# Performance work log

Hardware: AMD Instinct MI355X
Metric: run time of the kernel (lower is better)

The kernel has to match this reference:

```python
import jax, jax.numpy as jnp
import numpy as np

N_NODES = 50000
N_EDGES = 200000
NODE_DIM = 160     # node feat dim (divisible by 5 per wrapper slicing)
EDGE_DIM = 64      # latent edge feat dim
RAW_EDGE_DIM = 8   # raw geometric edge attributes
HID = 256          # hidden dim of edge/node update MLPs
ENC_HID = 128      # hidden dim of EASP edge encoder
N_ITER = 3
ENC_IN = 2 * NODE_DIM + RAW_EDGE_DIM                 # 328
EDGE_IN = 2 * 2 * NODE_DIM + 2 * EDGE_DIM            # 768 (reattach -> factor 2)
MSG_IN = 2 * NODE_DIM + EDGE_DIM                     # 384 (reattach node + edge)


def _ln(x, g, b):
    mu = jnp.mean(x, axis=-1, keepdims=True)
    v = jnp.var(x, axis=-1, keepdims=True)
    return (x - mu) * jax.lax.rsqrt(v + 1e-5) * g + b


def setup_inputs() -> dict:
    key = jax.random.key(0)
    ks = jax.random.split(key, 24)

    def w(k, shape):
        return (jax.random.normal(k, shape, jnp.float32) / np.sqrt(shape[0])).astype(jnp.float32)

    return {
        'x': jax.random.normal(ks[0], (N_NODES, NODE_DIM), jnp.float32),
        'edge_attr': jax.random.normal(ks[1], (N_EDGES, RAW_EDGE_DIM), jnp.float32),
        # EASP edge encoder MLP
        'enc_W1': w(ks[2], (ENC_IN, ENC_HID)), 'enc_b1': jnp.zeros((ENC_HID,), jnp.float32),
        'enc_W2': w(ks[3], (ENC_HID, EDGE_DIM)), 'enc_b2': jnp.zeros((EDGE_DIM,), jnp.float32),
        # EdgeCNN edge update MLP
        'eW1': w(ks[4], (EDGE_IN, HID)), 'eb1': jnp.zeros((HID,), jnp.float32),
        'eW2': w(ks[5], (HID, EDGE_DIM)), 'eb2': jnp.zeros((EDGE_DIM,), jnp.float32),
        # AttentionNodeUpdateNet: per-edge message MLP + attention vector + node out
        'mW1': w(ks[6], (MSG_IN, HID)), 'mb1': jnp.zeros((HID,), jnp.float32),
        'att_v': w(ks[7], (HID,)),
        'nW1': w(ks[8], (HID, NODE_DIM)), 'nb1': jnp.zeros((NODE_DIM,), jnp.float32),
        # shared LayerNorms (ModuleList([layer]*n_iter) shares one layer)
        'ln_ng': jnp.ones((NODE_DIM,), jnp.float32), 'ln_nb': jnp.zeros((NODE_DIM,), jnp.float32),
        'ln_eg': jnp.ones((EDGE_DIM,), jnp.float32), 'ln_eb': jnp.zeros((EDGE_DIM,), jnp.float32),
        'edge_row': jax.random.randint(ks[9], (N_EDGES,), 0, N_NODES, jnp.int32),
        'edge_col': jax.random.randint(ks[10], (N_EDGES,), 0, N_NODES, jnp.int32),
    }


def reference(x, edge_attr, enc_W1, enc_b1, enc_W2, enc_b2, eW1, eb1, eW2, eb2,
              mW1, mb1, att_v, nW1, nb1, ln_ng, ln_nb, ln_eg, ln_eb,
              edge_row, edge_col):
    row, col = edge_row, edge_col
    # edge encoder: gather endpoints, encode raw edge attrs
    init_edge = jnp.concatenate([x[row], x[col], edge_attr], axis=1)  # [E, 328]
    init_edge = jnp.maximum(init_edge @ enc_W1 + enc_b1, 0.0) @ enc_W2 + enc_b2  # [E, 64]

    node_lat, edge_lat = x, init_edge
    for _ in range(N_ITER):
        nl = jnp.concatenate([x, node_lat], axis=1)            # reattach initial node feats [N, 320]
        el = jnp.concatenate([init_edge, edge_lat], axis=1)    # reattach initial edge feats [E, 128]
        # edge update: gather-concat-MLP
        e_in = jnp.concatenate([nl[row], nl[col], el], axis=1)  # [E, 768]
        new_edge = jnp.maximum(e_in @ eW1 + eb1, 0.0) @ eW2 + eb2  # [E, 64]
        # node update: per-edge message + segment-softmax attention + scatter agg
        msg = jnp.maximum(jnp.concatenate([nl[col], new_edge], axis=1) @ mW1 + mb1, 0.0)  # [E, 256]
        logit = jax.nn.leaky_relu(msg @ att_v, 0.2)             # [E]
        smax = jax.ops.segment_max(logit, row, num_segments=N_NODES)
        ex = jnp.exp(logit - smax[row])
        den = jax.ops.segment_sum(ex, row, num_segments=N_NODES)
        alpha = ex / (den[row] + 1e-16)
        agg = jax.ops.segment_sum(alpha[:, None] * msg, row, num_segments=N_NODES)  # [N, 256]
        new_node = agg @ nW1 + nb1                              # [N, 160]
        # residual skip + (shared) LayerNorm
        node_lat = _ln(x + new_node, ln_ng, ln_nb)
        edge_lat = _ln(init_edge + new_edge, ln_eg, ln_eb)
    return node_lat, edge_lat
```

## Files before the change

### kernel.cpp

```cpp
#include <hip/hip_runtime.h>
#include <stdint.h>

#define N_NODES 50000
#define N_EDGES 200000
#define SCAN_B 512

typedef __bf16 bf16_t;
typedef bf16_t bf16x8 __attribute__((ext_vector_type(8)));
typedef float f32x4 __attribute__((ext_vector_type(4)));

__device__ __forceinline__ float bf2f(ushort h) {
  union { unsigned int u; float f; } c; c.u = ((unsigned int)h) << 16; return c.f;
}
__device__ __forceinline__ ushort f2bf(float f) {
  union { float f; unsigned int u; } c; c.f = f;
  unsigned int r = (c.u >> 16) & 1u;
  c.u += 0x7fffu + r;
  return (ushort)(c.u >> 16);
}
__device__ __forceinline__ float wave_sum(float v) {
#pragma unroll
  for (int m = 32; m > 0; m >>= 1) v += __shfl_xor(v, m, 64);
  return v;
}

__global__ void detect_k(const ushort* x, unsigned int* flag) {
  int i = blockIdx.x * 256 + threadIdx.x;
  unsigned int cnt = 0;
  for (int j = i; j < 1000000; j += 64 * 256) {
    ushort v = x[j];
    if (((v & 0x7F80u) == 0x7F80u) && (v & 0x7Fu)) cnt++;
  }
  if (cnt) atomicAdd(flag, cnt);
}

__global__ void cvt_in_k(const void* src, ushort* dst, int n, const unsigned int* flag) {
  int i = blockIdx.x * 256 + threadIdx.x;
  if (i >= n) return;
  if (*flag >= 2) dst[i] = f2bf(((const float*)src)[i]);
  else            dst[i] = ((const ushort*)src)[i];
}

__global__ void cvt_eattr_k(const void* src, const int* perm, ushort* dst,
                            const unsigned int* flag) {
  int i = blockIdx.x * 256 + threadIdx.x;
  if (i >= N_EDGES * 8) return;
  int e = i >> 3, j = i & 7;
  size_t o = (size_t)perm[e] * 8 + j;
  if (*flag >= 2) dst[i] = f2bf(((const float*)src)[o]);
  else            dst[i] = ((const ushort*)src)[o];
}

__global__ void transpose2_k(const void* W, ushort* Bt, int k0, int Ksrc, int Kpad,
                             int Wstride, const unsigned int* flag) {
  int k = blockIdx.x * 256 + threadIdx.x;
  int n = blockIdx.y;
  if (k >= Kpad) return;
  ushort v = 0;
  if (k < Ksrc) {
    if (*flag >= 2) v = f2bf(((const float*)W)[(size_t)(k0 + k) * Wstride + n]);
    else            v = ((const ushort*)W)[(size_t)(k0 + k) * Wstride + n];
  }
  Bt[(size_t)n * Kpad + k] = v;
}

__global__ void hist_k(const int* row, int* deg) {
  int e = blockIdx.x * 256 + threadIdx.x;
  if (e < N_EDGES) atomicAdd(&deg[row[e]], 1);
}
__global__ void scan_blk_k(const int* deg, int* off, int* bsum, int n) {
  __shared__ int s[SCAN_B];
  int i = blockIdx.x * SCAN_B + threadIdx.x;
  int v = (i < n) ? deg[i] : 0;
  s[threadIdx.x] = v;
  __syncthreads();
  for (int o = 1; o < SCAN_B; o <<= 1) {
    int t = (threadIdx.x >= o) ? s[threadIdx.x - o] : 0;
    __syncthreads();
    s[threadIdx.x] += t;
    __syncthreads();
  }
  if (i < n) off[i] = s[threadIdx.x] - v;
  if (threadIdx.x == SCAN_B - 1) bsum[blockIdx.x] = s[SCAN_B - 1];
}
__global__ void scan_top_k(int* bsum, int nb) {
  __shared__ int s[128];
  int v = (threadIdx.x < nb) ? bsum[threadIdx.x] : 0;
  s[threadIdx.x] = v;
  __syncthreads();
  for (int o = 1; o < 128; o <<= 1) {
    int t = (threadIdx.x >= o) ? s[threadIdx.x - o] : 0;
    __syncthreads();
    s[threadIdx.x] += t;
    __syncthreads();
  }
  if (threadIdx.x < nb) bsum[threadIdx.x] = s[threadIdx.x] - v;
}
__global__ void scan_add_k(int* off, const int* bsum, int n) {
  int i = blockIdx.x * 256 + threadIdx.x;
  if (i < n) off[i] += bsum[i >> 9];
  if (i == 0) off[n] = N_EDGES;
}
__global__ void fill_k(const int* row, const int* off, int* cur, int* perm) {
  int e = blockIdx.x * 256 + threadIdx.x;
  if (e >= N_EDGES) return;
  int r = row[e];
  int p = off[r] + atomicAdd(&cur[r], 1);
  perm[p] = e;
}
__global__ void gather_rc_k(const int* row, const int* col, const int* perm,
                            int* rs, int* cs) {
  int e = blockIdx.x * 256 + threadIdx.x;
  if (e >= N_EDGES) return;
  int o = perm[e];
  rs[e] = row[o];
  cs[e] = col[o];
}

struct GemmP {
  const ushort* X;
  const ushort* L;
  const ushort* E2;
  const float*  Af;
  const int* row;
  const int* col;
  const ushort* Bt;
  const ushort* bias;
  const ushort* Cr;
  const ushort* Cc;
  long cst;
  ushort* outb;  long ob_stride;
  ushort* outb2; long ob2_stride;
  ushort* outS;  long oS_stride;
  int nsplit;
  float*  outf;  long of_stride;
  long e2s;
  int M, K, Nw;
  int swzn;
};

template <int MODE>
__device__ __forceinline__ uint4 load_a8(const GemmP& p, int e, int kg) {
  if (MODE == 0) {
    return *(const uint4*)(p.E2 + (size_t)e * p.e2s + kg);
  } else if (MODE == 5) {
    if (kg < 160) return *(const uint4*)(p.X + (size_t)e * 160 + kg);
    return *(const uint4*)(p.L + (size_t)e * 160 + (kg - 160));
  } else if (MODE == 7) {
    if (kg < 160) return *(const uint4*)(p.X + (size_t)e * 160 + kg);
    uint4 z; z.x = z.y = z.z = z.w = 0u; return z;
  } else if (MODE == 8) {
    if (kg < 8) return *(const uint4*)(p.E2 + (size_t)e * 8);
    uint4 z; z.x = z.y = z.z = z.w = 0u; return z;
  } else {
    const float* s = p.Af + (size_t)e * p.K + kg;
    f32x4 f0 = *(const f32x4*)s;
    f32x4 f1 = *(const f32x4*)(s + 4);
    union { ushort r[8]; uint4 u; } o;
    o.r[0] = f2bf(f0[0]); o.r[1] = f2bf(f0[1]); o.r[2] = f2bf(f0[2]); o.r[3] = f2bf(f0[3]);
    o.r[4] = f2bf(f1[0]); o.r[5] = f2bf(f1[1]); o.r[6] = f2bf(f1[2]); o.r[7] = f2bf(f1[3]);
    return o.u;
  }
}

template <int MODE, int CI, bool RELU, int NT, bool LNN>
__global__ __launch_bounds__(256) void gemm_k(GemmP p) {
  constexpr int BR = NT / 2;
  constexpr int NTC = NT * 16;
  constexpr int CIP = NTC + 8;
  __shared__ __align__(16) ushort smem[9216 + 1152 * NT];
  ushort* Asm = smem;
  ushort* Bsm = smem + 9216;
  const int t = threadIdx.x;
  const int w = t >> 6;
  const int l = t & 63;
  int m0, n0;
  if (p.swzn) {
    int b = blockIdx.x;
    int panel = (b & 7) + ((b >> 3) / p.swzn) * 8;
    int nb = (b >> 3) % p.swzn;
    if (panel * 128 >= p.M) return;
    m0 = panel * 128;
    n0 = nb * NTC;
  } else {
    m0 = blockIdx.y * 128;
    n0 = blockIdx.x * NTC;
  }

  const int srow = t >> 1;
  const int sph = (t & 1) << 5;
  int e = m0 + srow;
  if (e >= p.M) e = p.M - 1;

  int bn_[BR], bk_[BR];
#pragma unroll
  for (int j = 0; j < BR; j++) {
    int cid = j * 256 + t;
    bn_[j] = cid >> 3;
    bk_[j] = (cid & 7) << 3;
  }

  const int mq = l & 15;
  const int qd = l >> 4;

  uint4 ar[4];
  uint4 br[BR];
  auto load_tile = [&](int k0) {
#pragma unroll
    for (int j = 0; j < 4; j++)
      ar[j] = load_a8<MODE>(p, e, k0 + sph + j * 8);
#pragma unroll
    for (int j = 0; j < BR; j++)
      br[j] = *(const uint4*)(p.Bt + (size_t)(n0 + bn_[j]) * p.K + k0 + bk_[j]);
  };

  load_tile(0);

  f32x4 acc[2][NT] = {};
  if (CI) {
#pragma unroll
    for (int mt = 0; mt < 2; mt++) {
#pragma unroll
      for (int i = 0; i < 4; i++) {
        int r = m0 + w * 32 + mt * 16 + qd * 4 + i;
        if (r >= p.M) r = p.M - 1;
        const ushort* pc = p.Cc + (size_t)p.col[r] * p.cst + n0 + mq;
        const ushort* pr = nullptr;
        if (CI == 1) pr = p.Cr + (size_t)p.row[r] * p.cst + n0 + mq;
#pragma unroll
        for (int nt = 0; nt < NT; nt++) {
          float v = bf2f(pc[nt * 16]);
          if (CI == 1) v += bf2f(pr[nt * 16]);
          acc[mt][nt][i] = v;
        }
      }
    }
  }

  const int kiters = p.K >> 6;
  for (int kt = 0; kt < kiters; kt++) {
    __syncthreads();
#pragma unroll
    for (int j = 0; j < 4; j++)
      *(uint4*)&Asm[srow * 72 + sph + j * 8] = ar[j];
#pragma unroll
    for (int j = 0; j < BR; j++)
      *(uint4*)&Bsm[bn_[j] * 72 + bk_[j]] = br[j];
    if (kt + 1 < kiters) load_tile((kt + 1) << 6);
    __syncthreads();
#pragma unroll
    for (int ph = 0; ph < 2; ph++) {
      uint4 ra0 = *(const uint4*)&Asm[(w * 32 + mq) * 72 + ph * 32 + qd * 8];
      uint4 ra1 = *(const uint4*)&Asm[(w * 32 + 16 + mq) * 72 + ph * 32 + qd * 8];
      bf16x8 af0 = __builtin_bit_cast(bf16x8, ra0);
      bf16x8 af1 = __builtin_bit_cast(bf16x8, ra1);
#pragma unroll
      for (int nt = 0; nt < NT; nt++) {
        uint4 rb = *(const uint4*)&Bsm[(nt * 16 + mq) * 72 + ph * 32 + qd * 8];
        bf16x8 bfv = __builtin_bit_cast(bf16x8, rb);
        acc[0][nt] = __builtin_amdgcn_mfma_f32_16x16x32_bf16(af0, bfv, acc[0][nt], 0, 0, 0);
        acc[1][nt] = __builtin_amdgcn_mfma_f32_16x16x32_bf16(af1, bfv, acc[1][nt], 0, 0, 0);
      }
    }
  }

  if (MODE == 4) {
    if (LNN) {
#pragma unroll
      for (int mt = 0; mt < 2; mt++) {
#pragma unroll
        for (int i = 0; i < 4; i++) {
          int r = m0 + w * 32 + mt * 16 + qd * 4 + i;
          int rc = (r < p.M) ? r : p.M - 1;
          float vals[NT];
          float s = 0.0f;
#pragma unroll
          for (int nt = 0; nt < NT; nt++) {
            int c = n0 + nt * 16 + mq;
            float v = acc[mt][nt][i] + bf2f(p.bias[c]) +
                      bf2f(p.X[(size_t)rc * p.of_stride + c]);
            vals[nt] = v; s += v;
          }
#pragma unroll
          for (int m = 1; m <= 8; m <<= 1) s += __shfl_xor(s, m, 64);
          float mu = s * (1.0f / 160.0f);
          float ss = 0.0f;
#pragma unroll
          for (int nt = 0; nt < NT; nt++) { float d = vals[nt] - mu; ss += d * d; }
#pragma unroll
          for (int m = 1; m <= 8; m <<= 1) ss += __shfl_xor(ss, m, 64);
          float inv = rsqrtf(ss * (1.0f / 160.0f) + 1e-5f);
          if (r < p.M) {
#pragma unroll
            for (int nt = 0; nt < NT; nt++) {
              int c = n0 + nt * 16 + mq;
              float o = (vals[nt] - mu) * inv * bf2f(p.Cr[c]) + bf2f(p.Cc[c]);
              p.outb[(size_t)r * p.ob_stride + c] = f2bf(o);
            }
          }
        }
      }
    } else {
#pragma unroll
      for (int mt = 0; mt < 2; mt++) {
#pragma unroll
        for (int nt = 0; nt < NT; nt++) {
          int c = n0 + nt * 16 + mq;
          float bv = bf2f(p.bias[c]);
#pragma unroll
          for (int i = 0; i < 4; i++) {
            int r = m0 + w * 32 + mt * 16 + qd * 4 + i;
            if (r >= p.M) continue;
            float v = acc[mt][nt][i] + bv;
            if (RELU) v = fmaxf(v, 0.0f);
            p.outf[(size_t)r * p.of_stride + c] = v;
          }
        }
      }
    }
  } else {
    ushort* dst = p.outb;
    long dstr = p.ob_stride;
    int nb0 = n0;
    if (p.outS && n0 >= p.nsplit) { dst = p.outS; dstr = p.oS_stride; nb0 = n0 - p.nsplit; }
    __syncthreads();
    ushort* S = smem + w * (32 * CIP);
#pragma unroll
    for (int mt = 0; mt < 2; mt++) {
#pragma unroll
      for (int nt = 0; nt < NT; nt++) {
        float bv = bf2f(p.bias[n0 + nt * 16 + mq]);
#pragma unroll
        for (int i = 0; i < 4; i++) {
          float v = acc[mt][nt][i] + bv;
          if (RELU) v = fmaxf(v, 0.0f);
          S[(mt * 16 + qd * 4 + i) * CIP + nt * 16 + mq] = f2bf(v);
        }
      }
    }
    __syncthreads();
#pragma unroll
    for (int j = 0; j < NT; j++) {
      int flat = (j * 64 + l) * 8;
      int lr = flat / NTC, cc = flat % NTC;
      int r = m0 + w * 32 + lr;
      if (r < p.M) {
        uint4 v = *(const uint4*)&S[lr * CIP + cc];
        *(uint4*)(dst + (size_t)r * dstr + nb0 + cc) = v;
        if (p.outb2) *(uint4*)(p.outb2 + (size_t)r * p.ob2_stride + n0 + cc) = v;
      }
    }
  }
}

__global__ __launch_bounds__(512) void edge12_k(
    const ushort* el, const int* rs, const int* cs, const ushort* Prc,
    const ushort* BtWe, const ushort* eb1, const ushort* Bte2, const ushort* eb2,
    ushort* elw, int M) {
  __shared__ __align__(16) ushort smem[32768];
  ushort* Asm = smem;
  ushort* Bsm = smem + 9216;
  const int t = threadIdx.x;
  const int w = t >> 6;
  const int l = t & 63;
  const int m0 = blockIdx.x * 128;
  const int mq = l & 15;
  const int qd = l >> 4;

  const int arow = t >> 2;
  const int aph = (t & 3) << 4;
  int ea = m0 + arow;
  if (ea >= M) ea = M - 1;
  int bn_[4], bk_[4];
#pragma unroll
  for (int j = 0; j < 4; j++) {
    int cid = j * 512 + t;
    bn_[j] = cid >> 3;
    bk_[j] = (cid & 7) << 3;
  }

  uint4 ar[2], br[4];
  auto load_tile = [&](int k0) {
#pragma unroll
    for (int j = 0; j < 2; j++)
      ar[j] = *(const uint4*)(el + (size_t)ea * 128 + k0 + aph + j * 8);
#pragma unroll
    for (int j = 0; j < 4; j++)
      br[j] = *(const uint4*)(BtWe + (size_t)bn_[j] * 128 + k0 + bk_[j]);
  };
  load_tile(0);

  f32x4 acc[16] = {};
#pragma unroll
  for (int i = 0; i < 4; i++) {
    int r = m0 + w * 16 + qd * 4 + i;
    if (r >= M) r = M - 1;
    const ushort* pc = Prc + (size_t)cs[r] * 512 + 256 + mq;
    const ushort* pr = Prc + (size_t)rs[r] * 512 + mq;
#pragma unroll
    for (int nt = 0; nt < 16; nt++)
      acc[nt][i] = bf2f(pc[nt * 16]) + bf2f(pr[nt * 16]);
  }

#pragma unroll
  for (int kt = 0; kt < 2; kt++) {
    __syncthreads();
#pragma unroll
    for (int j = 0; j < 2; j++)
      *(uint4*)&Asm[arow * 72 + aph + j * 8] = ar[j];
#pragma unroll
    for (int j = 0; j < 4; j++)
      *(uint4*)&Bsm[bn_[j] * 72 + bk_[j]] = br[j];
    if (kt == 0) load_tile(64);
    __syncthreads();
#pragma unroll
    for (int ph = 0; ph < 2; ph++) {
      uint4 ra = *(const uint4*)&Asm[(w * 16 + mq) * 72 + ph * 32 + qd * 8];
      bf16x8 af = __builtin_bit_cast(bf16x8, ra);
#pragma unroll
      for (int nt = 0; nt < 16; nt++) {
        uint4 rb = *(const uint4*)&Bsm[(nt * 16 + mq) * 72 + ph * 32 + qd * 8];
        bf16x8 bfv = __builtin_bit_cast(bf16x8, rb);
        acc[nt] = __builtin_amdgcn_mfma_f32_16x16x32_bf16(af, bfv, acc[nt], 0, 0, 0);
      }
    }
  }

  __syncthreads();
  ushort* S = smem + w * 4096;
#pragma unroll
  for (int nt = 0; nt < 16; nt++) {
    float bv = bf2f(eb1[nt * 16 + mq]);
#pragma unroll
    for (int i = 0; i < 4; i++) {
      int row = qd * 4 + i;
      float v = fmaxf(acc[nt][i] + bv, 0.0f);
      int bcol = ((nt * 16 + mq) * 2) ^ ((row & 7) << 4);
      S[row * 256 + (bcol >> 1)] = f2bf(v);
    }
  }
  __syncthreads();

  f32x4 acc2[4] = {};
#pragma unroll
  for (int ks = 0; ks < 8; ks++) {
    int bco = ((ks * 32 + qd * 8) * 2) ^ ((mq & 7) << 4);
    uint4 ra2 = *(const uint4*)&S[mq * 256 + (bco >> 1)];
    bf16x8 af2 = __builtin_bit_cast(bf16x8, ra2);
#pragma unroll
    for (int nt2 = 0; nt2 < 4; nt2++) {
      uint4 rb2 = *(const uint4*)(Bte2 + (size_t)(nt2 * 16 + mq) * 256 + ks * 32 + qd * 8);
      bf16x8 bf2v = __builtin_bit_cast(bf16x8, rb2);
      acc2[nt2] = __builtin_amdgcn_mfma_f32_16x16x32_bf16(af2, bf2v, acc2[nt2], 0, 0, 0);
    }
  }
  __syncthreads();

  ushort* S2 = smem + w * 1152;
#pragma unroll
  for (int nt2 = 0; nt2 < 4; nt2++) {
    float bv2 = bf2f(eb2[nt2 * 16 + mq]);
#pragma unroll
    for (int i = 0; i < 4; i++)
      S2[(qd * 4 + i) * 72 + nt2 * 16 + mq] = f2bf(acc2[nt2][i] + bv2);
  }
  __syncthreads();
#pragma unroll
  for (int j = 0; j < 2; j++) {
    int flat = (j * 64 + l) * 8;
    int lr = flat >> 6, cc = flat & 63;
    int r = m0 + w * 16 + lr;
    if (r < M)
      *(uint4*)(elw + (size_t)r * 128 + 64 + cc) = *(const uint4*)&S2[lr * 72 + cc];
  }
}

__global__ void copy_u4_k(const uint4* s, uint4* d, int n) {
  int i = blockIdx.x * 256 + threadIdx.x;
  if (i < n) d[i] = s[i];
}

__global__ void agg_csr_k(const ushort* msg, const ushort* att, const int* off,
                          float* agg) {
  int n = blockIdx.x * 4 + (threadIdx.x >> 6);
  int l = threadIdx.x & 63;
  if (n >= N_NODES) return;
  const int s0 = off[n], s1 = off[n + 1];
  ushort4 av = *(const ushort4*)(att + l * 4);
  const float a0 = bf2f(av.x), a1 = bf2f(av.y), a2 = bf2f(av.z), a3 = bf2f(av.w);
  float maxl = -1e30f;
  for (int j = s0; j < s1; j++) {
    ushort4 m = *(const ushort4*)(msg + (size_t)j * 256 + l * 4);
    float d = bf2f(m.x) * a0 + bf2f(m.y) * a1 + bf2f(m.z) * a2 + bf2f(m.w) * a3;
    d = wave_sum(d);
    float lg = (d > 0.0f) ? d : 0.2f * d;
    maxl = fmaxf(maxl, lg);
  }
  float den = 0.0f;
  f32x4 acc = {0.0f, 0.0f, 0.0f, 0.0f};
  for (int j = s0; j < s1; j++) {
    ushort4 m = *(const ushort4*)(msg + (size_t)j * 256 + l * 4);
    float m0 = bf2f(m.x), m1 = bf2f(m.y), m2 = bf2f(m.z), m3 = bf2f(m.w);
    float d = m0 * a0 + m1 * a1 + m2 * a2 + m3 * a3;
    d = wave_sum(d);
    float lg = (d > 0.0f) ? d : 0.2f * d;
    float ex = __expf(lg - maxl);
    den += ex;
    acc[0] += ex * m0; acc[1] += ex * m1; acc[2] += ex * m2; acc[3] += ex * m3;
  }
  float inv = 1.0f / (den + 1e-16f);
  f32x4 o = {acc[0] * inv, acc[1] * inv, acc[2] * inv, acc[3] * inv};
  *(f32x4*)(agg + (size_t)n * 256 + l * 4) = o;
}

__global__ void ln_edge_k(const ushort* g, const ushort* b, ushort* el) {
  int e = blockIdx.x * 4 + (threadIdx.x >> 6);
  int l = threadIdx.x & 63;
  if (e >= N_EDGES) return;
  float v = bf2f(el[(size_t)e * 128 + l]) + bf2f(el[(size_t)e * 128 + 64 + l]);
  float mu = wave_sum(v) * (1.0f / 64.0f);
  float d = v - mu;
  float var = wave_sum(d * d) * (1.0f / 64.0f);
  float inv = rsqrtf(var + 1e-5f);
  el[(size_t)e * 128 + 64 + l] = f2bf(d * inv * bf2f(g[l]) + bf2f(b[l]));
}

__global__ void out_node_k(const ushort* nlat, void* out, const unsigned int* flag) {
  int i = blockIdx.x * 256 + threadIdx.x;
  if (i >= N_NODES * 160) return;
  if (*flag >= 2) ((float*)out)[i] = bf2f(nlat[i]);
  else            ((ushort*)out)[i] = nlat[i];
}
__global__ void out_edge_k(const ushort* el, const int* perm, void* out,
                           const unsigned int* flag) {
  int i = blockIdx.x * 256 + threadIdx.x;
  if (i >= N_EDGES * 64) return;
  int e = i >> 6, c = i & 63;
  ushort v = el[(size_t)e * 128 + 64 + c];
  size_t o = (size_t)N_NODES * 160 + (size_t)perm[e] * 64 + c;
  if (*flag >= 2) ((float*)out)[o] = bf2f(v);
  else            ((ushort*)out)[o] = v;
}

extern "C" void kernel_launch(void* const* d_in, const int* in_sizes, int n_in,
                              void* d_out, int out_size, void* d_ws, size_t ws_size,
                              hipStream_t stream) {
  const void* x_r     = d_in[0];
  const void* eattr_r = d_in[1];
  const void* encW1   = d_in[2];
  const void* encb1_r = d_in[3];
  const void* encW2   = d_in[4];
  const void* encb2_r = d_in[5];
  const void* eW1     = d_in[6];
  const void* eb1_r   = d_in[7];
  const void* eW2     = d_in[8];
  const void* eb2_r   = d_in[9];
  const void* mW1     = d_in[10];
  const void* mb1_r   = d_in[11];
  const void* attv_r  = d_in[12];
  const void* nW1     = d_in[13];
  const void* nb1_r   = d_in[14];
  const void* lnng_r  = d_in[15];
  const void* lnnb_r  = d_in[16];
  const void* lneg_r  = d_in[17];
  const void* lneb_r  = d_in[18];
  const int* erow = (const int*)d_in[19];
  const int* ecol = (const int*)d_in[20];
  (void)in_sizes; (void)n_in;

  char* ws = (char*)d_ws;
  size_t off = 0;
  auto alloc = [&](size_t bytes) -> void* {
    void* p = ws + off;
    off = (off + bytes + 511) & ~(size_t)511;
    return p;
  };
  ushort* hm   = (ushort*)alloc((size_t)N_EDGES * 256 * 2);
  ushort* el   = (ushort*)alloc((size_t)N_EDGES * 128 * 2);
  float*  agg  = (float*)alloc((size_t)N_NODES * 256 * 4);
  ushort* xc   = (ushort*)alloc((size_t)N_NODES * 160 * 2);
  ushort* nlat = (ushort*)alloc((size_t)N_NODES * 160 * 2);
  ushort* Qc   = (ushort*)alloc((size_t)N_NODES * 256 * 2);
  int* degcur  = (int*)alloc((size_t)2 * N_NODES * 4);
  int* offcsr  = (int*)alloc((size_t)(N_NODES + 1) * 4);
  int* perm    = (int*)alloc((size_t)N_EDGES * 4);
  int* rs      = (int*)alloc((size_t)N_EDGES * 4);
  int* cs      = (int*)alloc((size_t)N_EDGES * 4);
  int* bsum    = (int*)alloc((size_t)128 * 4);
  ushort* BtPe = (ushort*)alloc((size_t)256 * 192 * 2);
  ushort* BtWenc = (ushort*)alloc((size_t)128 * 64 * 2);
  ushort* BtE2 = (ushort*)alloc((size_t)64 * 128 * 2);
  ushort* BtPQ = (ushort*)alloc((size_t)768 * 320 * 2);
  ushort* BtWe = (ushort*)alloc((size_t)256 * 128 * 2);
  ushort* Bte2 = (ushort*)alloc((size_t)64 * 256 * 2);
  ushort* BtWm = (ushort*)alloc((size_t)256 * 64 * 2);
  ushort* Btn1 = (ushort*)alloc((size_t)160 * 256 * 2);
  ushort* pool = (ushort*)alloc((size_t)4096 * 2);
  unsigned int* flag = (unsigned int*)alloc(64);
  ushort* msg = hm;
  ushort* eac  = (ushort*)agg;
  ushort* Penc = (ushort*)((char*)agg + (size_t)N_EDGES * 8 * 2);
  ushort* Prc  = (ushort*)agg;
  ushort* zb   = pool + 2048;

  ushort* encb1c = pool;        ushort* encb2c = pool + 128;
  ushort* eb1c   = pool + 192;  ushort* eb2c   = pool + 448;
  ushort* mb1c   = pool + 512;  ushort* attvc  = pool + 768;
  ushort* nb1c   = pool + 1024; ushort* lnngc  = pool + 1184;
  ushort* lnnbc  = pool + 1344; ushort* lnegc  = pool + 1504;
  ushort* lnebc  = pool + 1568;

  if (off > ws_size) {
    hipMemsetAsync(d_out, 0, (size_t)out_size * 2, stream);
    return;
  }

  hipMemsetAsync(flag, 0, 64, stream);
  hipMemsetAsync(pool, 0, 4096 * 2, stream);
  hipMemsetAsync(degcur, 0, (size_t)2 * N_NODES * 4, stream);

  detect_k<<<64, 256, 0, stream>>>((const ushort*)x_r, flag);

  {
    int* deg = degcur;
    int* cur = degcur + N_NODES;
    const int nb = (N_NODES + SCAN_B - 1) / SCAN_B;
    hist_k<<<(N_EDGES + 255) / 256, 256, 0, stream>>>(erow, deg);
    scan_blk_k<<<nb, SCAN_B, 0, stream>>>(deg, offcsr, bsum, N_NODES);
    scan_top_k<<<1, 128, 0, stream>>>(bsum, nb);
    scan_add_k<<<(N_NODES + 255) / 256, 256, 0, stream>>>(offcsr, bsum, N_NODES);
    fill_k<<<(N_EDGES + 255) / 256, 256, 0, stream>>>(erow, offcsr, cur, perm);
    gather_rc_k<<<(N_EDGES + 255) / 256, 256, 0, stream>>>(erow, ecol, perm, rs, cs);
  }

  cvt_in_k<<<(N_NODES * 160 + 255) / 256, 256, 0, stream>>>(x_r, xc, N_NODES * 160, flag);
  cvt_eattr_k<<<(N_EDGES * 8 + 255) / 256, 256, 0, stream>>>(eattr_r, perm, eac, flag);
  cvt_in_k<<<1, 256, 0, stream>>>(encb1_r, encb1c, 128, flag);
  cvt_in_k<<<1, 256, 0, stream>>>(encb2_r, encb2c, 64, flag);
  cvt_in_k<<<1, 256, 0, stream>>>(eb1_r, eb1c, 256, flag);
  cvt_in_k<<<1, 256, 0, stream>>>(eb2_r, eb2c, 64, flag);
  cvt_in_k<<<1, 256, 0, stream>>>(mb1_r, mb1c, 256, flag);
  cvt_in_k<<<1, 256, 0, stream>>>(attv_r, attvc, 256, flag);
  cvt_in_k<<<1, 256, 0, stream>>>(nb1_r, nb1c, 160, flag);
  cvt_in_k<<<1, 256, 0, stream>>>(lnng_r, lnngc, 160, flag);
  cvt_in_k<<<1, 256, 0, stream>>>(lnnb_r, lnnbc, 160, flag);
  cvt_in_k<<<1, 256, 0, stream>>>(lneg_r, lnegc, 64, flag);
  cvt_in_k<<<1, 256, 0, stream>>>(lneb_r, lnebc, 64, flag);

  transpose2_k<<<dim3(1, 128), 256, 0, stream>>>(encW1, BtPe,             0, 160, 192, 128, flag);
  transpose2_k<<<dim3(1, 128), 256, 0, stream>>>(encW1, BtPe + 128 * 192, 160, 160, 192, 128, flag);
  transpose2_k<<<dim3(1, 128), 256, 0, stream>>>(encW1, BtWenc,           320, 8, 64, 128, flag);
  transpose2_k<<<dim3(1, 64), 256, 0, stream>>>(encW2, BtE2, 0, 128, 128, 64, flag);
  transpose2_k<<<dim3(2, 256), 256, 0, stream>>>(eW1, BtPQ,             0, 320, 320, 256, flag);
  transpose2_k<<<dim3(2, 256), 256, 0, stream>>>(eW1, BtPQ + 256 * 320, 320, 320, 320, 256, flag);
  transpose2_k<<<dim3(2, 256), 256, 0, stream>>>(mW1, BtPQ + 512 * 320, 0, 320, 320, 256, flag);
  transpose2_k<<<dim3(1, 256), 256, 0, stream>>>(eW1, BtWe, 640, 128, 128, 256, flag);
  transpose2_k<<<dim3(1, 64), 256, 0, stream>>>(eW2, Bte2, 0, 256, 256, 64, flag);
  transpose2_k<<<dim3(1, 256), 256, 0, stream>>>(mW1, BtWm, 320, 64, 64, 256, flag);
  transpose2_k<<<dim3(1, 160), 256, 0, stream>>>(nW1, Btn1, 0, 256, 256, 160, flag);

  copy_u4_k<<<(N_NODES * 160 / 8 + 255) / 256, 256, 0, stream>>>(
      (const uint4*)xc, (uint4*)nlat, N_NODES * 160 / 8);

  const int gE = (N_EDGES + 127) / 128;
  const int gN = (N_NODES + 127) / 128;
  const int gN8 = 8 * ((gN + 7) / 8);
  const int gE8 = 8 * ((gE + 7) / 8);

  {
    GemmP p{};
    p.X = xc; p.Bt = BtPe; p.bias = zb;
    p.outb = Penc; p.ob_stride = 256;
    p.M = N_NODES; p.K = 192; p.Nw = 256; p.swzn = 2;
    gemm_k<7, 0, false, 8, false><<<gN8 * 2, 256, 0, stream>>>(p);
  }
  {
    GemmP p{};
    p.E2 = eac; p.row = rs; p.col = cs;
    p.Cr = Penc; p.Cc = Penc + 128; p.cst = 256;
    p.Bt = BtWenc; p.bias = encb1c;
    p.outb = hm; p.ob_stride = 128;
    p.M = N_EDGES; p.K = 64; p.Nw = 128;
    gemm_k<8, 1, true, 8, false><<<dim3(1, gE), 256, 0, stream>>>(p);
  }
  {
    GemmP p{};
    p.E2 = hm; p.e2s = 128; p.Bt = BtE2; p.bias = encb2c;
    p.outb = el; p.ob_stride = 128;
    p.outb2 = el + 64; p.ob2_stride = 128;
    p.M = N_EDGES; p.K = 128; p.Nw = 64;
    gemm_k<0, 0, false, 4, false><<<dim3(1, gE), 256, 0, stream>>>(p);
  }

  for (int it = 0; it < 3; it++) {
    {
      GemmP p{};
      p.X = xc; p.L = nlat; p.Bt = BtPQ; p.bias = zb;
      p.outb = Prc; p.ob_stride = 512;
      p.outS = Qc; p.oS_stride = 256; p.nsplit = 512;
      p.M = N_NODES; p.K = 320; p.Nw = 768; p.swzn = 6;
      gemm_k<5, 0, false, 8, false><<<gN8 * 6, 256, 0, stream>>>(p);
    }
    edge12_k<<<gE, 512, 0, stream>>>(el, rs, cs, Prc, BtWe, eb1c, Bte2, eb2c,
                                     el, N_EDGES);
    {
      GemmP p{};
      p.E2 = el + 64; p.e2s = 128; p.row = rs; p.col = cs;
      p.Cc = Qc; p.cst = 256;
      p.Bt = BtWm; p.bias = mb1c;
      p.outb = msg; p.ob_stride = 256;
      p.M = N_EDGES; p.K = 64; p.Nw = 256; p.swzn = 2;
      gemm_k<0, 2, true, 8, false><<<gE8 * 2, 256, 0, stream>>>(p);
    }
    ln_edge_k<<<N_EDGES / 4, 256, 0, stream>>>(lnegc, lnebc, el);
    agg_csr_k<<<(N_NODES + 3) / 4, 256, 0, stream>>>(msg, attvc, offcsr, agg);
    {
      GemmP p{};
      p.Af = agg; p.Bt = Btn1; p.bias = nb1c;
      p.X = xc; p.of_stride = 160;
      p.Cr = lnngc; p.Cc = lnnbc;
      p.outb = nlat; p.ob_stride = 160;
      p.M = N_NODES; p.K = 256; p.Nw = 160;
      gemm_k<4, 0, false, 10, true><<<dim3(1, gN), 256, 0, stream>>>(p);
    }
  }

  out_node_k<<<(N_NODES * 160 + 255) / 256, 256, 0, stream>>>(nlat, d_out, flag);
  out_edge_k<<<(N_EDGES * 64 + 255) / 256, 256, 0, stream>>>(el, perm, d_out, flag);
  (void)out_size;
}
```

Measured before the change: 1.979 ms.

## Fuse message GEMM into edge MLP kernel and drop block swizzle

Merges the per-edge message GEMM (new_edge @ mW1 plus the gathered Q[col] term, bias and ReLU) into the edge-update kernel. The freshly computed new_edge tile is reused from shared memory instead of being written out and re-read by a separate GEMM launch. The XOR swizzle patterns are adjusted and the Q[col] gathers are issued early to overlap with the second GEMM. It also removes the panel block-swizzle in the generic GEMM and goes back to a plain 2D grid, which may hurt L2 reuse. The fused kernel needs more accumulator registers (16 extra f32x4), which may lower occupancy.

Measured after the change: 1.894 ms. -4.3%, faster.

```diff
diff --git a/kernel.cpp b/kernel.cpp
--- a/kernel.cpp
+++ b/kernel.cpp
@@ -136,7 +136,6 @@
   float*  outf;  long of_stride;
   long e2s;
   int M, K, Nw;
-  int swzn;
 };
 
 template <int MODE>
@@ -174,18 +173,8 @@
   const int t = threadIdx.x;
   const int w = t >> 6;
   const int l = t & 63;
-  int m0, n0;
-  if (p.swzn) {
-    int b = blockIdx.x;
-    int panel = (b & 7) + ((b >> 3) / p.swzn) * 8;
-    int nb = (b >> 3) % p.swzn;
-    if (panel * 128 >= p.M) return;
-    m0 = panel * 128;
-    n0 = nb * NTC;
-  } else {
-    m0 = blockIdx.y * 128;
-    n0 = blockIdx.x * NTC;
-  }
+  const int m0 = blockIdx.y * 128;
+  const int n0 = blockIdx.x * NTC;
 
   const int srow = t >> 1;
   const int sph = (t & 1) << 5;
@@ -353,10 +342,11 @@
   }
 }
 
-__global__ __launch_bounds__(512) void edge12_k(
+__global__ __launch_bounds__(512) void edge123_k(
     const ushort* el, const int* rs, const int* cs, const ushort* Prc,
-    const ushort* BtWe, const ushort* eb1, const ushort* Bte2, const ushort* eb2,
-    ushort* elw, int M) {
+    const ushort* Qc, const ushort* BtWe, const ushort* eb1,
+    const ushort* Bte2, const ushort* eb2, const ushort* BtWm,
+    const ushort* mb1, ushort* elw, ushort* msg, int M) {
   __shared__ __align__(16) ushort smem[32768];
   ushort* Asm = smem;
   ushort* Bsm = smem + 9216;
@@ -435,17 +425,26 @@
     for (int i = 0; i < 4; i++) {
       int row = qd * 4 + i;
       float v = fmaxf(acc[nt][i] + bv, 0.0f);
-      int bcol = ((nt * 16 + mq) * 2) ^ ((row & 7) << 4);
-      S[row * 256 + (bcol >> 1)] = f2bf(v);
-    }
+      S[row * 256 + ((nt * 16 + mq) ^ ((row & 15) << 3))] = f2bf(v);
+    }
+  }
+
+  f32x4 acc3[16];
+#pragma unroll
+  for (int i = 0; i < 4; i++) {
+    int r = m0 + w * 16 + qd * 4 + i;
+    if (r >= M) r = M - 1;
+    const ushort* pq = Qc + (size_t)cs[r] * 256 + mq;
+#pragma unroll
+    for (int nt = 0; nt < 16; nt++)
+      acc3[nt][i] = bf2f(pq[nt * 16]);
   }
   __syncthreads();
 
   f32x4 acc2[4] = {};
 #pragma unroll
   for (int ks = 0; ks < 8; ks++) {
-    int bco = ((ks * 32 + qd * 8) * 2) ^ ((mq & 7) << 4);
-    uint4 ra2 = *(const uint4*)&S[mq * 256 + (bco >> 1)];
+    uint4 ra2 = *(const uint4*)&S[mq * 256 + ((ks * 32 + qd * 8) ^ ((mq & 15) << 3))];
     bf16x8 af2 = __builtin_bit_cast(bf16x8, ra2);
 #pragma unroll
     for (int nt2 = 0; nt2 < 4; nt2++) {
@@ -456,22 +455,63 @@
   }
   __syncthreads();
 
-  ushort* S2 = smem + w * 1152;
+  ushort* Sne = smem + w * 1024;
 #pragma unroll
   for (int nt2 = 0; nt2 < 4; nt2++) {
     float bv2 = bf2f(eb2[nt2 * 16 + mq]);
 #pragma unroll
-    for (int i = 0; i < 4; i++)
-      S2[(qd * 4 + i) * 72 + nt2 * 16 + mq] = f2bf(acc2[nt2][i] + bv2);
+    for (int i = 0; i < 4; i++) {
+      int row = qd * 4 + i;
+      Sne[row * 64 + ((nt2 * 16 + mq) ^ ((row & 7) << 3))] = f2bf(acc2[nt2][i] + bv2);
+    }
   }
   __syncthreads();
-#pragma unroll
-  for (int j = 0; j < 2; j++) {
+
+  {
+    int row = l >> 2;
+    int r = m0 + w * 16 + row;
+#pragma unroll
+    for (int h = 0; h < 2; h++) {
+      int cbase = (l & 3) * 16 + h * 8;
+      if (r < M)
+        *(uint4*)(elw + (size_t)r * 128 + 64 + cbase) =
+            *(const uint4*)&Sne[row * 64 + (cbase ^ ((row & 7) << 3))];
+    }
+  }
+
+#pragma unroll
+  for (int ph = 0; ph < 2; ph++) {
+    uint4 ra3 = *(const uint4*)&Sne[mq * 64 + ((ph * 32 + qd * 8) ^ ((mq & 7) << 3))];
+    bf16x8 af3 = __builtin_bit_cast(bf16x8, ra3);
+#pragma unroll
+    for (int nt = 0; nt < 16; nt++) {
+      uint4 rb3 = *(const uint4*)(BtWm + (size_t)(nt * 16 + mq) * 64 + ph * 32 + qd * 8);
+      bf16x8 bf3v = __builtin_bit_cast(bf16x8, rb3);
+      acc3[nt] = __builtin_amdgcn_mfma_f32_16x16x32_bf16(af3, bf3v, acc3[nt], 0, 0, 0);
+    }
+  }
+  __syncthreads();
+
+#pragma unroll
+  for (int nt = 0; nt < 16; nt++) {
+    float bv3 = bf2f(mb1[nt * 16 + mq]);
+#pragma unroll
+    for (int i = 0; i < 4; i++) {
+      int row = qd * 4 + i;
+      float v = fmaxf(acc3[nt][i] + bv3, 0.0f);
+      S[row * 256 + ((nt * 16 + mq) ^ ((row & 15) << 3))] = f2bf(v);
+    }
+  }
+  __syncthreads();
+#pragma unroll
+  for (int j = 0; j < 8; j++) {
     int flat = (j * 64 + l) * 8;
-    int lr = flat >> 6, cc = flat & 63;
-    int r = m0 + w * 16 + lr;
-    if (r < M)
-      *(uint4*)(elw + (size_t)r * 128 + 64 + cc) = *(const uint4*)&S2[lr * 72 + cc];
+    int row = flat >> 8, col = flat & 255;
+    int r = m0 + w * 16 + row;
+    if (r < M) {
+      uint4 v = *(const uint4*)&S[row * 256 + (col ^ ((row & 15) << 3))];
+      *(uint4*)(msg + (size_t)r * 256 + col) = v;
+    }
   }
 }
 
@@ -664,15 +704,13 @@
 
   const int gE = (N_EDGES + 127) / 128;
   const int gN = (N_NODES + 127) / 128;
-  const int gN8 = 8 * ((gN + 7) / 8);
-  const int gE8 = 8 * ((gE + 7) / 8);
 
   {
     GemmP p{};
     p.X = xc; p.Bt = BtPe; p.bias = zb;
     p.outb = Penc; p.ob_stride = 256;
-    p.M = N_NODES; p.K = 192; p.Nw = 256; p.swzn = 2;
-    gemm_k<7, 0, false, 8, false><<<gN8 * 2, 256, 0, stream>>>(p);
+    p.M = N_NODES; p.K = 192; p.Nw = 256;
+    gemm_k<7, 0, false, 8, false><<<dim3(2, gN), 256, 0, stream>>>(p);
   }
   {
     GemmP p{};
@@ -698,20 +736,11 @@
       p.X = xc; p.L = nlat; p.Bt = BtPQ; p.bias = zb;
       p.outb = Prc; p.ob_stride = 512;
       p.outS = Qc; p.oS_stride = 256; p.nsplit = 512;
-      p.M = N_NODES; p.K = 320; p.Nw = 768; p.swzn = 6;
-      gemm_k<5, 0, false, 8, false><<<gN8 * 6, 256, 0, stream>>>(p);
-    }
-    edge12_k<<<gE, 512, 0, stream>>>(el, rs, cs, Prc, BtWe, eb1c, Bte2, eb2c,
-                                     el, N_EDGES);
-    {
-      GemmP p{};
-      p.E2 = el + 64; p.e2s = 128; p.row = rs; p.col = cs;
-      p.Cc = Qc; p.cst = 256;
-      p.Bt = BtWm; p.bias = mb1c;
-      p.outb = msg; p.ob_stride = 256;
-      p.M = N_EDGES; p.K = 64; p.Nw = 256; p.swzn = 2;
-      gemm_k<0, 2, true, 8, false><<<gE8 * 2, 256, 0, stream>>>(p);
-    }
+      p.M = N_NODES; p.K = 320; p.Nw = 768;
+      gemm_k<5, 0, false, 8, false><<<dim3(6, gN), 256, 0, stream>>>(p);
+    }
+    edge123_k<<<gE, 512, 0, stream>>>(el, rs, cs, Prc, Qc, BtWe, eb1c,
+                                      Bte2, eb2c, BtWm, mb1c, el, msg, N_EDGES);
     ln_edge_k<<<N_EDGES / 4, 256, 0, stream>>>(lnegc, lnebc, el);
     agg_csr_k<<<(N_NODES + 3) / 4, 256, 0, stream>>>(msg, attvc, offcsr, agg);
     {
```
